# Kernel tuning notes

Measured on AMD Instinct MI355X. Metric: run time of the kernel, lower is better.

## Reference

```python
import jax, jax.numpy as jnp
import numpy as np

N_QUBITS = 10
BATCH = 16384
Q_DEPTH = 2


def _apply_1q_shared(state, U, q):
    # state: [B, 2, 2, ..., 2]; U: [2, 2] complex, acting on wire q
    state = jnp.moveaxis(state, 1 + q, -1)
    state = jnp.einsum('b...i,ji->b...j', state, U)
    return jnp.moveaxis(state, -1, 1 + q)


def _apply_ry_batched(state, angles, q):
    # per-sample RY(angle) on wire q; angles: [B] float
    c = jnp.cos(angles * 0.5).astype(jnp.complex64)
    s = jnp.sin(angles * 0.5).astype(jnp.complex64)
    U = jnp.stack([jnp.stack([c, -s], -1), jnp.stack([s, c], -1)], -2)  # [B,2,2]
    state = jnp.moveaxis(state, 1 + q, -1)
    state = jnp.einsum('b...i,bji->b...j', state, U)
    return jnp.moveaxis(state, -1, 1 + q)


def _rot_matrix(phi, theta, omega):
    # PennyLane Rot = RZ(omega) @ RY(theta) @ RZ(phi)
    c = jnp.cos(theta * 0.5)
    s = jnp.sin(theta * 0.5)
    m00 = jnp.exp(-0.5j * (phi + omega)) * c
    m01 = -jnp.exp(0.5j * (phi - omega)) * s
    m10 = jnp.exp(-0.5j * (phi - omega)) * s
    m11 = jnp.exp(0.5j * (phi + omega)) * c
    return jnp.stack([jnp.stack([m00, m01]), jnp.stack([m10, m11])]).astype(jnp.complex64)


def _apply_cnot(state, c, t):
    st = jnp.moveaxis(state, (1 + c, 1 + t), (1, 2))  # [B, ctrl, tgt, ...]
    st = jnp.stack([st[:, 0], st[:, 1, ::-1]], axis=1)  # flip target where ctrl=1
    return jnp.moveaxis(st, (1, 2), (1 + c, 1 + t))


def setup_inputs() -> dict:
    key = jax.random.key(0)
    k1, k2 = jax.random.split(key)
    x = jax.random.uniform(k1, (BATCH, N_QUBITS), dtype=jnp.float32) * np.pi
    q_weights = 0.01 * jax.random.normal(k2, (Q_DEPTH, N_QUBITS, 3), dtype=jnp.float32)
    return {"x": x, "q_weights": q_weights}


def reference(x, q_weights) -> jnp.ndarray:
    B, n = x.shape
    L = q_weights.shape[0]
    # |0...0> statevector, batched: [B] + [2]*n (axis q <-> wire q, wire 0 most significant)
    state = jnp.zeros((B, 2 ** n), jnp.complex64).at[:, 0].set(1.0)
    state = state.reshape((B,) + (2,) * n)
    # AngleEmbedding(rotation='Y')
    for q in range(n):
        state = _apply_ry_batched(state, x[:, q], q)
    # StronglyEntanglingLayers: Rot on each wire, then ring of CNOTs with range (l % (n-1)) + 1
    for l in range(L):
        for q in range(n):
            U = _rot_matrix(q_weights[l, q, 0], q_weights[l, q, 1], q_weights[l, q, 2])
            state = _apply_1q_shared(state, U, q)
        r = (l % (n - 1)) + 1
        for q in range(n):
            state = _apply_cnot(state, q, (q + r) % n)
    probs = jnp.abs(state.reshape(B, 2 ** n)) ** 2  # [B, 2^n]
    bits = (np.arange(2 ** n)[:, None] >> (n - 1 - np.arange(n))[None, :]) & 1
    signs = jnp.asarray(1.0 - 2.0 * bits, jnp.float32)  # [2^n, n], PauliZ eigenvalues
    return (probs @ signs).astype(jnp.float32)  # [B, n] expvals
```

## Files before the change

kernel.cpp:

```cpp
#include <hip/hip_runtime.h>

#define DEVINL __device__ __forceinline__

struct GC { int laneXor, regXor, rowL, rowR; };
struct Circ { GC g[20]; int sgnL[10], sgnR[10]; };

constexpr Circ build_circ() {
    Circ c{};
    unsigned A[10] = {};
    for (int i = 0; i < 10; ++i) A[i] = 1u << i;
    for (int w = 0; w < 10; ++w) {
        int pos = 9 - w;
        unsigned m = 1u << pos;
        c.g[w] = GC{ int(m >> 4), int(m & 15u), int(m >> 4), int(m & 15u) };
    }
    for (int q = 0; q < 10; ++q) { int pc = 9 - q, pt = 9 - ((q + 1) % 10); A[pt] ^= A[pc]; }
    unsigned M[10] = {}, Inv[10] = {};
    for (int i = 0; i < 10; ++i) { M[i] = A[i]; Inv[i] = 1u << i; }
    for (int col = 0; col < 10; ++col) {
        int piv = col;
        while (!((M[piv] >> col) & 1u)) ++piv;
        unsigned tm = M[col]; M[col] = M[piv]; M[piv] = tm;
        unsigned ti = Inv[col]; Inv[col] = Inv[piv]; Inv[piv] = ti;
        for (int r = 0; r < 10; ++r)
            if (r != col && ((M[r] >> col) & 1u)) { M[r] ^= M[col]; Inv[r] ^= Inv[col]; }
    }
    for (int w = 0; w < 10; ++w) {
        int pos = 9 - w;
        unsigned m = 0;
        for (int i = 0; i < 10; ++i) m |= ((Inv[i] >> pos) & 1u) << i;
        unsigned row = A[pos];
        c.g[10 + w] = GC{ int(m >> 4), int(m & 15u), int(row >> 4), int(row & 15u) };
    }
    for (int q = 0; q < 10; ++q) { int pc = 9 - q, pt = 9 - ((q + 2) % 10); A[pt] ^= A[pc]; }
    for (int q = 0; q < 10; ++q) { unsigned row = A[9 - q]; c.sgnL[q] = int(row >> 4); c.sgnR[q] = int(row & 15u); }
    return c;
}

constexpr Circ CC = build_circ();

DEVINL float csign(float v, int s) {
    return __int_as_float(__float_as_int(v) ^ (s << 31));
}

template<int XOR>
DEVINL float lx(float v, int lane) {
    int x = __float_as_int(v);
    int r;
    if constexpr (XOR == 1)      r = __builtin_amdgcn_update_dpp(0, x, 0xB1, 0xF, 0xF, true);
    else if constexpr (XOR == 2) r = __builtin_amdgcn_update_dpp(0, x, 0x4E, 0xF, 0xF, true);
    else if constexpr (XOR == 3) r = __builtin_amdgcn_update_dpp(0, x, 0x1B, 0xF, 0xF, true);
    else if constexpr (XOR < 32) r = __builtin_amdgcn_ds_swizzle(x, 0x1F | (XOR << 10));
    else                         r = __builtin_amdgcn_ds_bpermute((lane ^ XOR) << 2, x);
    return __int_as_float(r);
}

template<int G>
DEVINL void gates(float (&ar)[16], float (&ai)[16], const float* mats, int lane) {
    if constexpr (G < 20) {
        constexpr GC gc = CC.g[G];
        float fAr = mats[G * 4 + 0];
        float fAi = mats[G * 4 + 1];
        float fBr = mats[G * 4 + 2];
        float fBi = mats[G * 4 + 3];
        int sL = __popc(unsigned(lane & gc.rowL)) & 1;
        fAi = csign(fAi, sL);
        fBr = csign(fBr, sL);
        float br_[16], bi_[16];
        if constexpr (gc.laneXor == 0) {
            #pragma unroll
            for (int r = 0; r < 16; ++r) { br_[r] = ar[r ^ gc.regXor]; bi_[r] = ai[r ^ gc.regXor]; }
        } else {
            #pragma unroll
            for (int r = 0; r < 16; ++r) {
                br_[r] = lx<gc.laneXor>(ar[r ^ gc.regXor], lane);
                bi_[r] = lx<gc.laneXor>(ai[r ^ gc.regXor], lane);
            }
        }
        #pragma unroll
        for (int r = 0; r < 16; ++r) {
            const int cR = __builtin_popcount(unsigned(gc.rowR & r)) & 1;
            float a_r = ar[r], a_i = ai[r], b_r = br_[r], b_i = bi_[r];
            float nr, ni;
            if (!cR) {
                nr = fAr * a_r - fAi * a_i + fBr * b_r - fBi * b_i;
                ni = fAr * a_i + fAi * a_r + fBr * b_i + fBi * b_r;
            } else {
                nr = fAr * a_r + fAi * a_i - fBr * b_r - fBi * b_i;
                ni = fAr * a_i - fAi * a_r - fBr * b_i + fBi * b_r;
            }
            ar[r] = nr; ai[r] = ni;
        }
        gates<G + 1>(ar, ai, mats, lane);
    }
}

__global__ __launch_bounds__(256) void qsim(const float* __restrict__ x,
                                            const float* __restrict__ qw,
                                            float* __restrict__ out, int B) {
    __shared__ float sm[80];
    {
        int g = threadIdx.x;
        if (g < 20) {
            float phi = qw[g * 3 + 0], th = qw[g * 3 + 1], om = qw[g * 3 + 2];
            float c = cosf(0.5f * th), s = sinf(0.5f * th);
            float apo = 0.5f * (phi + om), amo = 0.5f * (phi - om);
            sm[g * 4 + 0] =  cosf(apo) * c;
            sm[g * 4 + 1] = -sinf(apo) * c;
            sm[g * 4 + 2] = -cosf(amo) * s;
            sm[g * 4 + 3] = -sinf(amo) * s;
        }
    }
    __syncthreads();

    int lane = threadIdx.x & 63;
    int b = __builtin_amdgcn_readfirstlane(blockIdx.x * 4 + (threadIdx.x >> 6));
    if (b >= B) return;

    const float* xb = x + b * 10;
    float f0r[10], f0i[10], f1r[10], f1i[10];
    #pragma unroll
    for (int w = 0; w < 10; ++w) {
        float h = 0.5f * xb[w];
        float s = __sinf(h), c = __cosf(h);
        float m0 = sm[w * 4 + 0], m1 = sm[w * 4 + 1], m2 = sm[w * 4 + 2], m3 = sm[w * 4 + 3];
        f0r[w] =  m0 * c + m2 * s;
        f0i[w] =  m1 * c + m3 * s;
        f1r[w] = -m2 * c + m0 * s;
        f1i[w] =  m3 * c - m1 * s;
    }

    float lfr, lfi;
    {
        int bit = lane & 1;
        lfr = bit ? f1r[5] : f0r[5];
        lfi = bit ? f1i[5] : f0i[5];
    }
    #pragma unroll
    for (int jj = 1; jj < 6; ++jj) {
        int w = 5 - jj;
        int bit = (lane >> jj) & 1;
        float pr = bit ? f1r[w] : f0r[w];
        float pi = bit ? f1i[w] : f0i[w];
        float nr = lfr * pr - lfi * pi;
        float ni = lfr * pi + lfi * pr;
        lfr = nr; lfi = ni;
    }
    float t01r[4], t01i[4], t23r[4], t23i[4];
    #pragma unroll
    for (int v = 0; v < 4; ++v) {
        float ar9 = (v & 1) ? f1r[9] : f0r[9], ai9 = (v & 1) ? f1i[9] : f0i[9];
        float ar8 = (v >> 1) ? f1r[8] : f0r[8], ai8 = (v >> 1) ? f1i[8] : f0i[8];
        t01r[v] = ar9 * ar8 - ai9 * ai8;
        t01i[v] = ar9 * ai8 + ai9 * ar8;
        float ar7 = (v & 1) ? f1r[7] : f0r[7], ai7 = (v & 1) ? f1i[7] : f0i[7];
        float ar6 = (v >> 1) ? f1r[6] : f0r[6], ai6 = (v >> 1) ? f1i[6] : f0i[6];
        t23r[v] = ar7 * ar6 - ai7 * ai6;
        t23i[v] = ar7 * ai6 + ai7 * ar6;
    }
    float g4r[4], g4i[4];
    #pragma unroll
    for (int v = 0; v < 4; ++v) {
        g4r[v] = lfr * t01r[v] - lfi * t01i[v];
        g4i[v] = lfr * t01i[v] + lfi * t01r[v];
    }
    float ar[16], ai[16];
    #pragma unroll
    for (int r = 0; r < 16; ++r) {
        ar[r] = g4r[r & 3] * t23r[r >> 2] - g4i[r & 3] * t23i[r >> 2];
        ai[r] = g4r[r & 3] * t23i[r >> 2] + g4i[r & 3] * t23r[r >> 2];
    }

    gates<10>(ar, ai, sm, lane);

    float prob[16];
    #pragma unroll
    for (int r = 0; r < 16; ++r) prob[r] = ar[r] * ar[r] + ai[r] * ai[r];

    float e[10];
    #pragma unroll
    for (int q = 0; q < 10; ++q) {
        float t = 0.f;
        #pragma unroll
        for (int r = 0; r < 16; ++r) {
            const int neg = __builtin_popcount(unsigned(CC.sgnR[q] & r)) & 1;
            t = neg ? (t - prob[r]) : (t + prob[r]);
        }
        int sl = __popc(unsigned(lane & CC.sgnL[q])) & 1;
        e[q] = csign(t, sl);
    }
    #pragma unroll
    for (int q = 0; q < 10; ++q) {
        e[q] += lx<1>(e[q], lane);
        e[q] += lx<2>(e[q], lane);
        e[q] += lx<4>(e[q], lane);
        e[q] += lx<8>(e[q], lane);
        e[q] += lx<16>(e[q], lane);
        e[q] += lx<32>(e[q], lane);
    }
    float v = e[0];
    #pragma unroll
    for (int q = 1; q < 10; ++q) v = (lane == q) ? e[q] : v;
    if (lane < 10) out[b * 10 + lane] = v;
}

extern "C" void kernel_launch(void* const* d_in, const int* in_sizes, int n_in,
                              void* d_out, int out_size, void* d_ws, size_t ws_size,
                              hipStream_t stream) {
    const float* x  = (const float*)d_in[0];
    const float* qw = (const float*)d_in[1];
    float* out = (float*)d_out;
    int B = in_sizes[0] / 10;
    int blocks = (B + 3) / 4;
    hipLaunchKernelGGL(qsim, dim3(blocks), dim3(256), 0, stream, x, qw, out, B);
}
```

Before: 95.78 us.

## Factor second-layer Rot into diagonal phases and scaled RY, use Walsh-Hadamard for expvals

The second layer's Rot gates are decomposed into diagonal RZ phases, which are folded into the product-state construction, and RY rotations rescaled by 1/cos so that each gate becomes a single FMA per amplitude with a signed tangent. The PauliZ expectation sums are computed with a 16-point Walsh-Hadamard butterfly instead of ten separate signed sums. DPP lane swaps are replaced by ds_swizzle. This cuts ALU work in the gate loop, at the cost of dividing by cos(theta/2), which is numerically fragile if that value is near zero, and of possibly slower swizzle-based cross-lane exchanges.

```diff
diff --git a/kernel.cpp b/kernel.cpp
--- a/kernel.cpp
+++ b/kernel.cpp
@@ -39,33 +39,49 @@
 
 constexpr Circ CC = build_circ();
 
-DEVINL float csign(float v, int s) {
-    return __int_as_float(__float_as_int(v) ^ (s << 31));
+static_assert(CC.g[10].rowL == 31 && CC.g[10].rowR == 15, "w0 row");
+static_assert(CC.g[11].rowL == 48 && CC.g[11].rowR == 0,  "w1 row");
+static_assert(CC.g[12].rowL == 56 && CC.g[12].rowR == 0,  "w2 row");
+static_assert(CC.g[13].rowL == 60 && CC.g[13].rowR == 0,  "w3 row");
+static_assert(CC.g[14].rowL == 62 && CC.g[14].rowR == 0,  "w4 row");
+static_assert(CC.g[15].rowL == 63 && CC.g[15].rowR == 0,  "w5 row");
+static_assert(CC.g[16].rowL == 63 && CC.g[16].rowR == 8,  "w6 row");
+static_assert(CC.g[17].rowL == 63 && CC.g[17].rowR == 12, "w7 row");
+static_assert(CC.g[18].rowL == 63 && CC.g[18].rowR == 14, "w8 row");
+static_assert(CC.g[19].rowL == 63 && CC.g[19].rowR == 15, "w9 row");
+
+DEVINL float csw(float v, int sw) {
+    return __int_as_float(__float_as_int(v) ^ sw);
 }
 
 template<int XOR>
 DEVINL float lx(float v, int lane) {
     int x = __float_as_int(v);
     int r;
-    if constexpr (XOR == 1)      r = __builtin_amdgcn_update_dpp(0, x, 0xB1, 0xF, 0xF, true);
-    else if constexpr (XOR == 2) r = __builtin_amdgcn_update_dpp(0, x, 0x4E, 0xF, 0xF, true);
-    else if constexpr (XOR == 3) r = __builtin_amdgcn_update_dpp(0, x, 0x1B, 0xF, 0xF, true);
-    else if constexpr (XOR < 32) r = __builtin_amdgcn_ds_swizzle(x, 0x1F | (XOR << 10));
-    else                         r = __builtin_amdgcn_ds_bpermute((lane ^ XOR) << 2, x);
+    if constexpr (XOR < 32) r = __builtin_amdgcn_ds_swizzle(x, 0x1F | (XOR << 10));
+    else                    r = __builtin_amdgcn_ds_bpermute((lane ^ XOR) << 2, x);
     return __int_as_float(r);
 }
 
+DEVINL void wf(const float* sm, float xw, int w,
+               float& a0r, float& a0i, float& a1r, float& a1i) {
+    float h = 0.5f * xw;
+    float s = __sinf(h), c = __cosf(h);
+    float m0 = sm[w * 4 + 0], m1 = sm[w * 4 + 1], m2 = sm[w * 4 + 2], m3 = sm[w * 4 + 3];
+    a0r =  m0 * c + m2 * s;
+    a0i =  m1 * c + m3 * s;
+    a1r = -m2 * c + m0 * s;
+    a1i =  m3 * c - m1 * s;
+}
+
 template<int G>
-DEVINL void gates(float (&ar)[16], float (&ai)[16], const float* mats, int lane) {
+DEVINL void rygates(float (&ar)[16], float (&ai)[16], const float* sm, int lane,
+                    const int (&sw)[10]) {
     if constexpr (G < 20) {
         constexpr GC gc = CC.g[G];
-        float fAr = mats[G * 4 + 0];
-        float fAi = mats[G * 4 + 1];
-        float fBr = mats[G * 4 + 2];
-        float fBi = mats[G * 4 + 3];
-        int sL = __popc(unsigned(lane & gc.rowL)) & 1;
-        fAi = csign(fAi, sL);
-        fBr = csign(fBr, sL);
+        constexpr int w = G - 10;
+        float t  = sm[40 + w * 4 + 1];
+        float tt = csw(t, sw[w]);
         float br_[16], bi_[16];
         if constexpr (gc.laneXor == 0) {
             #pragma unroll
@@ -79,19 +95,11 @@
         }
         #pragma unroll
         for (int r = 0; r < 16; ++r) {
-            const int cR = __builtin_popcount(unsigned(gc.rowR & r)) & 1;
-            float a_r = ar[r], a_i = ai[r], b_r = br_[r], b_i = bi_[r];
-            float nr, ni;
-            if (!cR) {
-                nr = fAr * a_r - fAi * a_i + fBr * b_r - fBi * b_i;
-                ni = fAr * a_i + fAi * a_r + fBr * b_i + fBi * b_r;
-            } else {
-                nr = fAr * a_r + fAi * a_i - fBr * b_r - fBi * b_i;
-                ni = fAr * a_i - fAi * a_r - fBr * b_i + fBi * b_r;
-            }
-            ar[r] = nr; ai[r] = ni;
-        }
-        gates<G + 1>(ar, ai, mats, lane);
+            const bool sR = __builtin_popcount(unsigned(gc.rowR & r)) & 1;
+            if (sR) { ar[r] = fmaf( tt, br_[r], ar[r]); ai[r] = fmaf( tt, bi_[r], ai[r]); }
+            else    { ar[r] = fmaf(-tt, br_[r], ar[r]); ai[r] = fmaf(-tt, bi_[r], ai[r]); }
+        }
+        rygates<G + 1>(ar, ai, sm, lane, sw);
     }
 }
 
@@ -101,7 +109,7 @@
     __shared__ float sm[80];
     {
         int g = threadIdx.x;
-        if (g < 20) {
+        if (g < 10) {
             float phi = qw[g * 3 + 0], th = qw[g * 3 + 1], om = qw[g * 3 + 2];
             float c = cosf(0.5f * th), s = sinf(0.5f * th);
             float apo = 0.5f * (phi + om), amo = 0.5f * (phi - om);
@@ -109,6 +117,14 @@
             sm[g * 4 + 1] = -sinf(apo) * c;
             sm[g * 4 + 2] = -cosf(amo) * s;
             sm[g * 4 + 3] = -sinf(amo) * s;
+        } else if (g < 20) {
+            int w = g - 10;
+            float phi = qw[g * 3 + 0], th = qw[g * 3 + 1];
+            float c = cosf(0.5f * th), s = sinf(0.5f * th);
+            sm[40 + w * 4 + 0] = c;
+            sm[40 + w * 4 + 1] = s / c;
+            sm[40 + w * 4 + 2] = cosf(0.5f * phi);
+            sm[40 + w * 4 + 3] = -sinf(0.5f * phi);
         }
     }
     __syncthreads();
@@ -116,48 +132,81 @@
     int lane = threadIdx.x & 63;
     int b = __builtin_amdgcn_readfirstlane(blockIdx.x * 4 + (threadIdx.x >> 6));
     if (b >= B) return;
-
     const float* xb = x + b * 10;
-    float f0r[10], f0i[10], f1r[10], f1i[10];
-    #pragma unroll
-    for (int w = 0; w < 10; ++w) {
-        float h = 0.5f * xb[w];
-        float s = __sinf(h), c = __cosf(h);
-        float m0 = sm[w * 4 + 0], m1 = sm[w * 4 + 1], m2 = sm[w * 4 + 2], m3 = sm[w * 4 + 3];
-        f0r[w] =  m0 * c + m2 * s;
-        f0i[w] =  m1 * c + m3 * s;
-        f1r[w] = -m2 * c + m0 * s;
-        f1i[w] =  m3 * c - m1 * s;
+
+    int l = lane;
+    int p48 = (l >> 4) ^ (l >> 5);
+    int p56 = p48 ^ (l >> 3);
+    int p60 = p56 ^ (l >> 2);
+    int p62 = p60 ^ (l >> 1);
+    int p63 = p62 ^ l;
+    int p31 = p63 ^ (l >> 5);
+    int s48 = p48 << 31, s56 = p56 << 31, s60 = p60 << 31;
+    int s62 = p62 << 31, s63 = p63 << 31, s31 = p31 << 31;
+    int sw[10] = { s31, s48, s56, s60, s62, s63, s63, s63, s63, s63 };
+
+    float t01r[4], t01i[4], t23r[4], t23i[4];
+    {
+        float a0r, a0i, a1r, a1i, b0r, b0i, b1r, b1i;
+        wf(sm, xb[9], 9, a0r, a0i, a1r, a1i);
+        wf(sm, xb[8], 8, b0r, b0i, b1r, b1i);
+        t01r[0] = a0r * b0r - a0i * b0i;  t01i[0] = a0r * b0i + a0i * b0r;
+        t01r[1] = a1r * b0r - a1i * b0i;  t01i[1] = a1r * b0i + a1i * b0r;
+        t01r[2] = a0r * b1r - a0i * b1i;  t01i[2] = a0r * b1i + a0i * b1r;
+        t01r[3] = a1r * b1r - a1i * b1i;  t01i[3] = a1r * b1i + a1i * b1r;
+        wf(sm, xb[7], 7, a0r, a0i, a1r, a1i);
+        wf(sm, xb[6], 6, b0r, b0i, b1r, b1i);
+        t23r[0] = a0r * b0r - a0i * b0i;  t23i[0] = a0r * b0i + a0i * b0r;
+        t23r[1] = a1r * b0r - a1i * b0i;  t23i[1] = a1r * b0i + a1i * b0r;
+        t23r[2] = a0r * b1r - a0i * b1i;  t23i[2] = a0r * b1i + a0i * b1r;
+        t23r[3] = a1r * b1r - a1i * b1i;  t23i[3] = a1r * b1i + a1i * b1r;
     }
 
     float lfr, lfi;
     {
-        int bit = lane & 1;
-        lfr = bit ? f1r[5] : f0r[5];
-        lfi = bit ? f1i[5] : f0i[5];
-    }
-    #pragma unroll
-    for (int jj = 1; jj < 6; ++jj) {
-        int w = 5 - jj;
-        int bit = (lane >> jj) & 1;
-        float pr = bit ? f1r[w] : f0r[w];
-        float pi = bit ? f1i[w] : f0i[w];
-        float nr = lfr * pr - lfi * pi;
-        float ni = lfr * pi + lfi * pr;
-        lfr = nr; lfi = ni;
-    }
-    float t01r[4], t01i[4], t23r[4], t23i[4];
-    #pragma unroll
-    for (int v = 0; v < 4; ++v) {
-        float ar9 = (v & 1) ? f1r[9] : f0r[9], ai9 = (v & 1) ? f1i[9] : f0i[9];
-        float ar8 = (v >> 1) ? f1r[8] : f0r[8], ai8 = (v >> 1) ? f1i[8] : f0i[8];
-        t01r[v] = ar9 * ar8 - ai9 * ai8;
-        t01i[v] = ar9 * ai8 + ai9 * ar8;
-        float ar7 = (v & 1) ? f1r[7] : f0r[7], ai7 = (v & 1) ? f1i[7] : f0i[7];
-        float ar6 = (v >> 1) ? f1r[6] : f0r[6], ai6 = (v >> 1) ? f1i[6] : f0i[6];
-        t23r[v] = ar7 * ar6 - ai7 * ai6;
-        t23i[v] = ar7 * ai6 + ai7 * ar6;
-    }
+        float ear = sm[40 + 1 * 4 + 2], eai = csw(sm[40 + 1 * 4 + 3], sw[1]);
+        #pragma unroll
+        for (int w = 2; w <= 5; ++w) {
+            float er = sm[40 + w * 4 + 2], ei = csw(sm[40 + w * 4 + 3], sw[w]);
+            float nr = ear * er - eai * ei;
+            float ni = ear * ei + eai * er;
+            ear = nr; eai = ni;
+        }
+        float sc = sm[40];
+        #pragma unroll
+        for (int w = 1; w < 10; ++w) sc *= sm[40 + w * 4];
+        lfr = ear * sc; lfi = eai * sc;
+        #pragma unroll
+        for (int jj = 0; jj < 6; ++jj) {
+            int w = 5 - jj;
+            float a0r, a0i, a1r, a1i;
+            wf(sm, xb[w], w, a0r, a0i, a1r, a1i);
+            int bit = (lane >> jj) & 1;
+            float pr = bit ? a1r : a0r;
+            float pi = bit ? a1i : a0i;
+            float nr = lfr * pr - lfi * pi;
+            float ni = lfr * pi + lfi * pr;
+            lfr = nr; lfi = ni;
+        }
+    }
+
+    float e6r = sm[40 + 6 * 4 + 2], e6i = csw(sm[40 + 6 * 4 + 3], sw[6]);
+    float e7r = sm[40 + 7 * 4 + 2], e7i = csw(sm[40 + 7 * 4 + 3], sw[7]);
+    float Pr_ = e6r * e7r - e6i * e7i, Pi_ = e6r * e7i + e6i * e7r;
+    float Qr_ = e6r * e7r + e6i * e7i, Qi_ = e6i * e7r - e6r * e7i;
+    float t23pr[4], t23pi[4];
+    t23pr[0] = t23r[0] * Pr_ - t23i[0] * Pi_;  t23pi[0] = t23r[0] * Pi_ + t23i[0] * Pr_;
+    t23pr[1] = t23r[1] * Qr_ - t23i[1] * Qi_;  t23pi[1] = t23r[1] * Qi_ + t23i[1] * Qr_;
+    t23pr[2] = t23r[2] * Pr_ + t23i[2] * Pi_;  t23pi[2] = t23i[2] * Pr_ - t23r[2] * Pi_;
+    t23pr[3] = t23r[3] * Qr_ + t23i[3] * Qi_;  t23pi[3] = t23i[3] * Qr_ - t23r[3] * Qi_;
+
+    float e0r = sm[40 + 0 * 4 + 2], e0i = csw(sm[40 + 0 * 4 + 3], sw[0]);
+    float e9r = sm[40 + 9 * 4 + 2], e9i = csw(sm[40 + 9 * 4 + 3], sw[9]);
+    float e8r = sm[40 + 8 * 4 + 2], e8i = csw(sm[40 + 8 * 4 + 3], sw[8]);
+    float ebr = e0r * e9r - e0i * e9i, ebi = e0r * e9i + e0i * e9r;
+    float G0r = e8r * ebr - e8i * ebi, G0i = e8r * ebi + e8i * ebr;
+    float G1r = e8r * ebr + e8i * ebi, G1i = e8i * ebr - e8r * ebi;
+
     float g4r[4], g4i[4];
     #pragma unroll
     for (int v = 0; v < 4; ++v) {
@@ -167,27 +216,37 @@
     float ar[16], ai[16];
     #pragma unroll
     for (int r = 0; r < 16; ++r) {
-        ar[r] = g4r[r & 3] * t23r[r >> 2] - g4i[r & 3] * t23i[r >> 2];
-        ai[r] = g4r[r & 3] * t23i[r >> 2] + g4i[r & 3] * t23r[r >> 2];
-    }
-
-    gates<10>(ar, ai, sm, lane);
-
-    float prob[16];
-    #pragma unroll
-    for (int r = 0; r < 16; ++r) prob[r] = ar[r] * ar[r] + ai[r] * ai[r];
+        float tr = g4r[r & 3] * t23pr[r >> 2] - g4i[r & 3] * t23pi[r >> 2];
+        float ti = g4r[r & 3] * t23pi[r >> 2] + g4i[r & 3] * t23pr[r >> 2];
+        float gr = (r & 1) ? G1r : G0r;
+        float gi = (r & 1) ? G1i : G0i;
+        if (__builtin_popcount(unsigned(r & 14)) & 1) gi = -gi;
+        ar[r] = tr * gr - ti * gi;
+        ai[r] = tr * gi + ti * gr;
+    }
+
+    rygates<10>(ar, ai, sm, lane, sw);
+
+    float wv[16];
+    #pragma unroll
+    for (int r = 0; r < 16; ++r) wv[r] = ar[r] * ar[r] + ai[r] * ai[r];
+    #pragma unroll
+    for (int bS = 1; bS < 16; bS <<= 1) {
+        #pragma unroll
+        for (int r = 0; r < 16; ++r) {
+            if (!(r & bS)) {
+                float xv = wv[r], yv = wv[r | bS];
+                wv[r]      = xv + yv;
+                wv[r | bS] = xv - yv;
+            }
+        }
+    }
 
     float e[10];
     #pragma unroll
     for (int q = 0; q < 10; ++q) {
-        float t = 0.f;
-        #pragma unroll
-        for (int r = 0; r < 16; ++r) {
-            const int neg = __builtin_popcount(unsigned(CC.sgnR[q] & r)) & 1;
-            t = neg ? (t - prob[r]) : (t + prob[r]);
-        }
-        int sl = __popc(unsigned(lane & CC.sgnL[q])) & 1;
-        e[q] = csign(t, sl);
+        int slq = __popc(unsigned(lane & CC.sgnL[q])) & 1;
+        e[q] = csw(wv[CC.sgnR[q]], slq << 31);
     }
     #pragma unroll
     for (int q = 0; q < 10; ++q) {
```

New measurement: 91.06 us. -4.9%, faster.
